# Kernel optimization log

Measured on AMD Instinct MI355X. Metric: run time of the kernel, lower is better.

## Reference

```python
import jax, jax.numpy as jnp
import numpy as np

S = 64.0
M = 0.5
COS_M = float(np.cos(M))
SIN_M = float(np.sin(M))
MM = float(np.sin(M) * M)
THRESHOLD = float(np.cos(np.pi - M))
B, D, V = 2048, 512, 100000


def setup_inputs() -> dict:
    key = jax.random.key(0)
    k1, k2, k3 = jax.random.split(key, 3)
    embeddings = jax.random.normal(k1, (B, D), dtype=jnp.float32)
    labels = jax.random.randint(k2, (B,), 0, V, dtype=jnp.int64)
    # xavier_uniform for [V, D]: limit = sqrt(6/(fan_in+fan_out))
    limit = float(np.sqrt(6.0 / (D + V)))
    weight = jax.random.uniform(k3, (V, D), minval=-limit, maxval=limit, dtype=jnp.float32)
    return {"embeddings": embeddings, "labels": labels, "weight": weight}


def _l2norm(x, axis):
    # matches F.normalize(p=2, eps=1e-12)
    n = jnp.linalg.norm(x, axis=axis, keepdims=True)
    return x / jnp.maximum(n, 1e-12)


def reference(embeddings, labels, weight):
    e = _l2norm(embeddings, axis=1)          # [B, D]
    w = _l2norm(weight, axis=1)              # [V, D]
    cos_theta = jnp.clip(e @ w.T, -1.0, 1.0)  # [B, V]
    sin_theta = jnp.sqrt(jnp.clip(1.0 - cos_theta * cos_theta, 0.0, 1.0))
    cos_theta_m = cos_theta * COS_M - sin_theta * SIN_M
    cos_theta_m = jnp.where(cos_theta > THRESHOLD, cos_theta_m, cos_theta - MM)
    logits = cos_theta_m * S
    logp = jax.nn.log_softmax(logits, axis=1)
    nll = -jnp.take_along_axis(logp, labels[:, None], axis=1)[:, 0]
    return jnp.mean(nll)
```

## Files before the change

kernel.cpp:

```cpp
#include <hip/hip_runtime.h>
#include <hip/hip_bf16.h>
#include <math.h>

#define B_ 2048
#define D_ 512
#define V_ 100000
#define BM 128
#define BN 128
#define NCT 782
#define NBLK (16 * NCT)
#define NBUF 3
#define RED_STRIDE 20

constexpr float S_SCALE = 64.0f;
constexpr float COS_M_ = 0.8775825618903728f;
constexpr float SIN_M_ = 0.479425538604203f;
constexpr float MM_    = 0.2397127693021015f;
constexpr float THRESH = -0.8775825618903728f;
constexpr float LOG2E  = 1.4426950408889634f;
constexpr float LN2    = 0.6931471805599453f;
constexpr float S2     = 64.0f * LOG2E;
constexpr float CMS2   = COS_M_ * S2;
constexpr float SINM_S2= SIN_M_ * S2;
constexpr float KS2    = SINM_S2 * SINM_S2;
constexpr float MMS2   = MM_ * S2;

constexpr float QS     = 508.0f;
constexpr float S8SQ   = QS * QS;
constexpr float S4_    = S8SQ * S8SQ;
constexpr float KS2C   = KS2 / S4_;
constexpr float CMS2C  = CMS2 / S8SQ;
constexpr float S2C    = S2 / S8SQ;
constexpr float THRESHI= THRESH * S8SQ;

constexpr float PA0  = -SINM_S2;
constexpr float PA1C = (SINM_S2 * 0.5f)    / S4_;
constexpr float PA2C = (SINM_S2 * 0.125f)  / (S4_ * S4_);
constexpr float PA3C = (SINM_S2 * 0.0625f) / (S4_ * S4_ * S4_);
constexpr float TH45I = 0.45f * S8SQ;

typedef __attribute__((ext_vector_type(8))) short short8;
typedef __attribute__((ext_vector_type(2))) float f32x2;
typedef __attribute__((ext_vector_type(4))) float f32x4;
typedef __attribute__((ext_vector_type(4))) int i32x4;

__device__ __forceinline__ unsigned short f2bf(float x) {
    __hip_bfloat16 h = __float2bfloat16(x);
    unsigned short u;
    __builtin_memcpy(&u, &h, 2);
    return u;
}

__device__ __forceinline__ void load_lds16(const void* g, void* l) {
    __builtin_amdgcn_global_load_lds(
        (const __attribute__((address_space(1))) unsigned int*)g,
        (__attribute__((address_space(3))) unsigned int*)l,
        16, 0, 0);
}

__device__ __forceinline__ int q8(float x) {
    float v = fminf(fmaxf(x * QS, -127.0f), 127.0f);
    return (int)rintf(v);
}
__device__ __forceinline__ unsigned int pk_i8x4(float x, float y, float z, float w) {
    return ((unsigned)q8(x) & 255u) | (((unsigned)q8(y) & 255u) << 8) |
           (((unsigned)q8(z) & 255u) << 16) | (((unsigned)q8(w) & 255u) << 24);
}

__global__ void k_norm_e(const float* __restrict__ e, unsigned short* __restrict__ ebf,
                         unsigned char* __restrict__ ebq, float* __restrict__ rne,
                         unsigned int* __restrict__ zbuf) {
    if (zbuf && blockIdx.x == 0) zbuf[threadIdx.x] = 0u;
    int row = blockIdx.x * 4 + (threadIdx.x >> 6);
    int lane = threadIdx.x & 63;
    const float4* src = (const float4*)(e + (size_t)row * D_);
    float4 a = src[lane];
    float4 b = src[lane + 64];
    float ss = a.x*a.x + a.y*a.y + a.z*a.z + a.w*a.w
             + b.x*b.x + b.y*b.y + b.z*b.z + b.w*b.w;
    #pragma unroll
    for (int d = 1; d < 64; d <<= 1) ss += __shfl_xor(ss, d, 64);
    float rn = 1.0f / fmaxf(sqrtf(ss), 1e-12f);
    ushort4* dst = (ushort4*)(ebf + (size_t)row * D_);
    dst[lane]      = make_ushort4(f2bf(a.x*rn), f2bf(a.y*rn), f2bf(a.z*rn), f2bf(a.w*rn));
    dst[lane + 64] = make_ushort4(f2bf(b.x*rn), f2bf(b.y*rn), f2bf(b.z*rn), f2bf(b.w*rn));
    if (ebq) {
        unsigned int* d8 = (unsigned int*)(ebq + (size_t)row * D_);
        d8[lane]      = pk_i8x4(a.x*rn, a.y*rn, a.z*rn, a.w*rn);
        d8[lane + 64] = pk_i8x4(b.x*rn, b.y*rn, b.z*rn, b.w*rn);
    }
    if (lane == 0) rne[row] = rn;
}

__global__ void k_norm_w(const float* __restrict__ w, float* __restrict__ rnw,
                         unsigned char* __restrict__ wbq) {
    int row = blockIdx.x * 4 + (threadIdx.x >> 6);
    int lane = threadIdx.x & 63;
    const float4* src = (const float4*)(w + (size_t)row * D_);
    float4 a = src[lane];
    float4 b = src[lane + 64];
    float ss = a.x*a.x + a.y*a.y + a.z*a.z + a.w*a.w
             + b.x*b.x + b.y*b.y + b.z*b.z + b.w*b.w;
    #pragma unroll
    for (int d = 1; d < 64; d <<= 1) ss += __shfl_xor(ss, d, 64);
    float rn = 1.0f / fmaxf(sqrtf(ss), 1e-12f);
    if (wbq) {
        unsigned int* d8 = (unsigned int*)(wbq + (size_t)row * D_);
        d8[lane]      = pk_i8x4(a.x*rn, a.y*rn, a.z*rn, a.w*rn);
        d8[lane + 64] = pk_i8x4(b.x*rn, b.y*rn, b.z*rn, b.w*rn);
    }
    if (lane == 0) rnw[row] = rn;
}

__global__ __launch_bounds__(256, 3) void k_gemm8(const unsigned char* __restrict__ ebq,
                                                  const unsigned char* __restrict__ wbq,
                                                  const unsigned char* __restrict__ zbuf,
                                                  float* __restrict__ partials) {
    const int id = blockIdx.x;
    const int wi = (id & 7) * (NBLK / 8) + (id >> 3);
    const int ct = wi >> 4, rt = wi & 15;
    const int row0 = rt * BM, n0 = ct * BN;
    const int tid = threadIdx.x, lane = tid & 63, wid = tid >> 6;
    const int wm = wid >> 1, wn = wid & 1;

    __shared__ __align__(16) unsigned char lds8[NBUF][16384];
    float* red = (float*)&lds8[0][0];

    i32x4 acc[4][4];
    #pragma unroll
    for (int i = 0; i < 4; ++i)
        #pragma unroll
        for (int j = 0; j < 4; ++j)
            acc[i][j] = (i32x4){0, 0, 0, 0};

    const int c_ = (lane & 3) ^ ((lane >> 3) & 3);
    const int r0s = wid * 16 + (lane >> 2);
    const unsigned char* gA0 = ebq + (size_t)(row0 + r0s) * D_ + c_ * 16;
    const unsigned char* gA1 = ebq + (size_t)(row0 + 64 + r0s) * D_ + c_ * 16;
    int gb0 = n0 + r0s, gb1 = n0 + 64 + r0s;
    const unsigned char* gB0 = (gb0 < V_) ? wbq + (size_t)gb0 * D_ + c_ * 16 : zbuf + c_ * 16;
    const unsigned char* gB1 = (gb1 < V_) ? wbq + (size_t)gb1 * D_ + c_ * 16 : zbuf + c_ * 16;
    const int lb = wid * 1024;

    auto STAGE = [&](int t) {
        unsigned char* Lb = &lds8[t % NBUF][0];
        const int off = t * 64;
        load_lds16(gA0 + off, Lb + lb);
        load_lds16(gA1 + off, Lb + 4096 + lb);
        load_lds16(gB0 + off, Lb + 8192 + lb);
        load_lds16(gB1 + off, Lb + 12288 + lb);
    };

    const int sA = ((lane >> 4) ^ ((lane >> 1) & 3)) & 3;
    int aoff[4], boff[4];
    #pragma unroll
    for (int mf = 0; mf < 4; ++mf)
        aoff[mf] = (wm * 64 + mf * 16 + (lane & 15)) * 64 + sA * 16;
    #pragma unroll
    for (int nf = 0; nf < 4; ++nf)
        boff[nf] = 8192 + (wn * 64 + nf * 16 + (lane & 15)) * 64 + sA * 16;

    STAGE(0);
    STAGE(1);
    for (int t = 0; t < 8; ++t) {
        if (t < 7) asm volatile("s_waitcnt vmcnt(4)\n\ts_barrier" ::: "memory");
        else       asm volatile("s_waitcnt vmcnt(0)\n\ts_barrier" ::: "memory");
        if (t + 2 < 8) STAGE(t + 2);

        const char* Lb = (const char*)&lds8[t % NBUF][0];
        i32x4 af[4], bq[4];
        #pragma unroll
        for (int mf = 0; mf < 4; ++mf) af[mf] = *(const i32x4*)(Lb + aoff[mf]);
        #pragma unroll
        for (int nf = 0; nf < 4; ++nf) bq[nf] = *(const i32x4*)(Lb + boff[nf]);
        #pragma unroll
        for (int mf = 0; mf < 4; ++mf)
            #pragma unroll
            for (int nf = 0; nf < 4; ++nf)
                acc[mf][nf] = __builtin_amdgcn_mfma_i32_16x16x64_i8(af[mf], bq[nf], acc[mf][nf], 0, 0, 0);
    }
    __syncthreads();

    const f32x2 k3 = {PA3C, PA3C}, k2 = {PA2C, PA2C}, k1 = {PA1C, PA1C},
                k0 = {PA0, PA0},   kc = {CMS2C, CMS2C};
    #pragma unroll
    for (int mf = 0; mf < 4; ++mf) {
        #pragma unroll
        for (int r = 0; r < 4; ++r) {
            float c0 = (float)acc[mf][0][r];
            float c1 = (float)acc[mf][1][r];
            float c2v = (float)acc[mf][2][r];
            float c3 = (float)acc[mf][3][r];
            float am = fmaxf(fmaxf(fabsf(c0), fabsf(c1)), fmaxf(fabsf(c2v), fabsf(c3)));
            float vsum;
            if (__builtin_expect(__any(am > TH45I), 0)) {
                float cs0 = c0, cs1 = c1, cs2 = c2v, cs3 = c3;
                vsum = 0.0f;
                float csa[4] = {cs0, cs1, cs2, cs3};
                #pragma unroll
                for (int nf = 0; nf < 4; ++nf) {
                    float ci = __builtin_amdgcn_fmed3f(csa[nf], -S8SQ, S8SQ);
                    float tt = fmaf(-ci, ci, S4_);
                    float sts = __builtin_amdgcn_sqrtf(tt * KS2C);
                    float lgm = fmaf(ci, CMS2C, -sts);
                    float lga = fmaf(ci, S2C, -MMS2);
                    float lg = (ci > THRESHI) ? lgm : lga;
                    vsum += __builtin_amdgcn_exp2f(lg);
                }
            } else {
                f32x2 ca = {c0, c1}, cb = {c2v, c3};
                f32x2 ua = ca * ca, ub = cb * cb;
                f32x2 pa = __builtin_elementwise_fma(ua, k3, k2);
                pa = __builtin_elementwise_fma(ua, pa, k1);
                pa = __builtin_elementwise_fma(ua, pa, k0);
                pa = __builtin_elementwise_fma(ca, kc, pa);
                f32x2 pb = __builtin_elementwise_fma(ub, k3, k2);
                pb = __builtin_elementwise_fma(ub, pb, k1);
                pb = __builtin_elementwise_fma(ub, pb, k0);
                pb = __builtin_elementwise_fma(cb, kc, pb);
                vsum = (__builtin_amdgcn_exp2f(pa.x) + __builtin_amdgcn_exp2f(pa.y))
                     + (__builtin_amdgcn_exp2f(pb.x) + __builtin_amdgcn_exp2f(pb.y));
            }
            int rowloc = wm * 64 + mf * 16 + (lane >> 4) * 4 + r;
            red[(wn * BM + rowloc) * RED_STRIDE + (lane & 15)] = vsum;
        }
    }
    __syncthreads();
    if (tid < BM) {
        const float4* p0 = (const float4*)(red + (size_t)tid * RED_STRIDE);
        const float4* p1 = (const float4*)(red + (size_t)(BM + tid) * RED_STRIDE);
        float s = 0.0f;
        #pragma unroll
        for (int q = 0; q < 4; ++q) {
            float4 u = p0[q], v = p1[q];
            s += (u.x + u.y) + (u.z + u.w) + (v.x + v.y) + (v.z + v.w);
        }
        partials[(size_t)ct * B_ + row0 + tid] = s;
    }
}

__device__ __forceinline__ int swz64(int row, int col) {
    return (row * 64 + col) ^ ((row & 7) << 3);
}
__global__ __launch_bounds__(256) void k_gemm_fb(const unsigned short* __restrict__ ebf,
                                                 const float* __restrict__ w,
                                                 const float* __restrict__ rnw,
                                                 float* __restrict__ partials) {
    const int rt = blockIdx.x, ct = blockIdx.y;
    const int row0 = rt * BM, n0 = ct * BN;
    const int tid = threadIdx.x, lane = tid & 63, wid = tid >> 6;
    const int wm = wid >> 1, wn = wid & 1;
    __shared__ __align__(16) unsigned short As[BM * 64];
    __shared__ __align__(16) unsigned short Bs[BN * 64];
    float* red = (float*)&As[0];
    f32x4 acc[4][4];
    #pragma unroll
    for (int i = 0; i < 4; ++i)
        #pragma unroll
        for (int j = 0; j < 4; ++j) acc[i][j] = (f32x4){0.f, 0.f, 0.f, 0.f};
    for (int ks = 0; ks < D_ / 64; ++ks) {
        const int kk = ks * 64;
        #pragma unroll
        for (int p = 0; p < 4; ++p) {
            int idx = p * 256 + tid;
            int r = idx >> 3, c = (idx & 7) * 8;
            *(uint4*)(As + swz64(r, c)) = *(const uint4*)(ebf + (size_t)(row0 + r) * D_ + kk + c);
        }
        #pragma unroll
        for (int p = 0; p < 4; ++p) {
            int idx = p * 256 + tid;
            int r = idx >> 3, c = (idx & 7) * 8;
            int gr = n0 + r;
            uint4 val = make_uint4(0, 0, 0, 0);
            if (gr < V_) {
                float rn = rnw[gr];
                const float4* src = (const float4*)(w + (size_t)gr * D_ + kk + c);
                float4 f0 = src[0], f1 = src[1];
                val.x = (unsigned)f2bf(f0.x*rn) | ((unsigned)f2bf(f0.y*rn) << 16);
                val.y = (unsigned)f2bf(f0.z*rn) | ((unsigned)f2bf(f0.w*rn) << 16);
                val.z = (unsigned)f2bf(f1.x*rn) | ((unsigned)f2bf(f1.y*rn) << 16);
                val.w = (unsigned)f2bf(f1.z*rn) | ((unsigned)f2bf(f1.w*rn) << 16);
            }
            *(uint4*)(Bs + swz64(r, c)) = val;
        }
        __syncthreads();
        #pragma unroll
        for (int kc = 0; kc < 2; ++kc) {
            const int kbase = kc * 32 + (lane >> 4) * 8;
            short8 af[4], bfr[4];
            #pragma unroll
            for (int mf = 0; mf < 4; ++mf) af[mf] = *(const short8*)(As + swz64(wm * 64 + mf * 16 + (lane & 15), kbase));
            #pragma unroll
            for (int nf = 0; nf < 4; ++nf) bfr[nf] = *(const short8*)(Bs + swz64(wn * 64 + nf * 16 + (lane & 15), kbase));
            #pragma unroll
            for (int mf = 0; mf < 4; ++mf)
                #pragma unroll
                for (int nf = 0; nf < 4; ++nf)
                    acc[mf][nf] = __builtin_amdgcn_mfma_f32_16x16x32_bf16(af[mf], bfr[nf], acc[mf][nf], 0, 0, 0);
        }
        __syncthreads();
    }
    const int vlim = V_ - n0;
    #pragma unroll
    for (int mf = 0; mf < 4; ++mf) {
        #pragma unroll
        for (int r = 0; r < 4; ++r) {
            float vsum = 0.0f;
            #pragma unroll
            for (int nf = 0; nf < 4; ++nf) {
                float c = acc[mf][nf][r];
                int coltile = wn * 64 + nf * 16 + (lane & 15);
                c = __builtin_amdgcn_fmed3f(c, -1.0f, 1.0f);
                float tt = fmaf(-c, c, 1.0f);
                float sts = __builtin_amdgcn_sqrtf(tt * KS2);
                float lgm = fmaf(c, CMS2, -sts);
                float lga = fmaf(c, S2, -MMS2);
                float lg = (c > THRESH) ? lgm : lga;
                lg = (coltile < vlim) ? lg : -INFINITY;
                vsum += __builtin_amdgcn_exp2f(lg);
            }
            int rowloc = wm * 64 + mf * 16 + (lane >> 4) * 4 + r;
            red[(wn * BM + rowloc) * RED_STRIDE + (lane & 15)] = vsum;
        }
    }
    __syncthreads();
    if (tid < BM) {
        const float4* p0 = (const float4*)(red + (size_t)tid * RED_STRIDE);
        const float4* p1 = (const float4*)(red + (size_t)(BM + tid) * RED_STRIDE);
        float s = 0.0f;
        #pragma unroll
        for (int q = 0; q < 4; ++q) {
            float4 u = p0[q], v = p1[q];
            s += (u.x + u.y) + (u.z + u.w) + (v.x + v.y) + (v.z + v.w);
        }
        partials[(size_t)ct * B_ + row0 + tid] = s;
    }
}

__device__ __forceinline__ int get_label(const int* lab32, int b) {
    bool is64 = true;
    #pragma unroll
    for (int i = 1; i < 16; i += 2) is64 = is64 && (lab32[i] == 0);
    return is64 ? (int)(((const long long*)lab32)[b]) : lab32[b];
}

__global__ void k_row(const float* __restrict__ e, const float* __restrict__ w,
                      const int* __restrict__ labels, const float* __restrict__ rne,
                      const float* __restrict__ rnw, const float* __restrict__ partials,
                      float* __restrict__ row_nll, float padcorr) {
    const int b = blockIdx.x;
    const int tid = threadIdx.x;

    float s = 0.0f;
    for (int ctn = tid; ctn < NCT; ctn += 256) s += partials[(size_t)ctn * B_ + b];
    #pragma unroll
    for (int d = 1; d < 64; d <<= 1) s += __shfl_xor(s, d, 64);
    __shared__ float ss_[4], sd_[4];
    if ((tid & 63) == 0) ss_[tid >> 6] = s;

    int lab = get_label(labels, b);
    const float* ep = e + (size_t)b * D_;
    const float* wp = w + (size_t)lab * D_;
    float dot = ep[tid] * wp[tid] + ep[tid + 256] * wp[tid + 256];
    #pragma unroll
    for (int d = 1; d < 64; d <<= 1) dot += __shfl_xor(dot, d, 64);
    if ((tid & 63) == 0) sd_[tid >> 6] = dot;
    __syncthreads();

    if (tid == 0) {
        float S = (ss_[0] + ss_[1]) + (ss_[2] + ss_[3]) - padcorr;
        float lse = __builtin_amdgcn_logf(S) * LN2;
        float c = (sd_[0] + sd_[1] + sd_[2] + sd_[3]) * rne[b] * rnw[lab];
        c = fminf(fmaxf(c, -1.0f), 1.0f);
        float st = sqrtf(fmaxf(1.0f - c * c, 0.0f));
        float cm = c * COS_M_ - st * SIN_M_;
        cm = (c > THRESH) ? cm : (c - MM_);
        row_nll[b] = lse - cm * S_SCALE;
    }
}

__global__ void k_mean(const float* __restrict__ row_nll, float* __restrict__ out) {
    int tid = threadIdx.x;
    float s = 0.0f;
    for (int i = tid; i < B_; i += 256) s += row_nll[i];
    #pragma unroll
    for (int d = 1; d < 64; d <<= 1) s += __shfl_xor(s, d, 64);
    __shared__ float sb[4];
    if ((tid & 63) == 0) sb[tid >> 6] = s;
    __syncthreads();
    if (tid == 0) out[0] = (sb[0] + sb[1] + sb[2] + sb[3]) / (float)B_;
}

extern "C" void kernel_launch(void* const* d_in, const int* in_sizes, int n_in,
                              void* d_out, int out_size, void* d_ws, size_t ws_size,
                              hipStream_t stream) {
    const float* e      = (const float*)d_in[0];
    const int*   labels = (const int*)d_in[1];
    const float* w      = (const float*)d_in[2];
    float* out = (float*)d_out;
    char* ws = (char*)d_ws;

    unsigned short* ebf = (unsigned short*)ws;
    float* rne          = (float*)(ws + 2097152);
    float* rnw          = (float*)(ws + 2105344);
    float* partials     = (float*)(ws + 2505344);
    float* row_nll      = (float*)(ws + 8911488);
    unsigned int* zbuf  = (unsigned int*)(ws + 8919680);
    unsigned char* ebq  = (unsigned char*)(ws + 8923776);
    unsigned char* wbq  = (unsigned char*)(ws + 9972352);
    const size_t NEED_PRE = 9972352 + (size_t)V_ * D_;

    const bool pre = ws_size >= NEED_PRE;
    const float padcorr = pre ? 96.0f * exp2f(-(float)SINM_S2) : 0.0f;

    k_norm_e<<<B_ / 4, 256, 0, stream>>>(e, ebf, pre ? ebq : nullptr, rne, pre ? zbuf : nullptr);
    k_norm_w<<<V_ / 4, 256, 0, stream>>>(w, rnw, pre ? wbq : nullptr);
    if (pre) {
        k_gemm8<<<NBLK, 256, 0, stream>>>(ebq, wbq, (const unsigned char*)zbuf, partials);
    } else {
        dim3 g3(B_ / BM, NCT);
        k_gemm_fb<<<g3, 256, 0, stream>>>(ebf, w, rnw, partials);
    }
    k_row<<<B_, 256, 0, stream>>>(e, w, labels, rne, rnw, partials, row_nll, padcorr);
    k_mean<<<1, 256, 0, stream>>>(row_nll, out);
}
```

Baseline: 194.1 us.

## Interleave split A/B prefetch with half-MFMA batches and raise wave priority

Splits the per-iteration global-to-LDS staging into separate A and B halves. Each half is issued between the LDS fragment reads and one half of the MFMA block, so memory traffic overlaps matrix work instead of all being issued at the top of the iteration. It also wraps each MFMA batch in s_setprio, adds sched_barrier fences, and adds a second workgroup barrier mid-iteration. The aim is better overlap of loads and MFMA issue across waves, at the cost of an extra barrier and explicit lgkmcnt waits per K step.

Result: no change. 194.4 us (+0.2%).

```diff
diff --git a/kernel.cpp b/kernel.cpp
--- a/kernel.cpp
+++ b/kernel.cpp
@@ -142,11 +142,15 @@
     const unsigned char* gB1 = (gb1 < V_) ? wbq + (size_t)gb1 * D_ + c_ * 16 : zbuf + c_ * 16;
     const int lb = wid * 1024;
 
-    auto STAGE = [&](int t) {
+    auto STAGE_A = [&](int t) {
         unsigned char* Lb = &lds8[t % NBUF][0];
         const int off = t * 64;
         load_lds16(gA0 + off, Lb + lb);
         load_lds16(gA1 + off, Lb + 4096 + lb);
+    };
+    auto STAGE_B = [&](int t) {
+        unsigned char* Lb = &lds8[t % NBUF][0];
+        const int off = t * 64;
         load_lds16(gB0 + off, Lb + 8192 + lb);
         load_lds16(gB1 + off, Lb + 12288 + lb);
     };
@@ -160,24 +164,44 @@
     for (int nf = 0; nf < 4; ++nf)
         boff[nf] = 8192 + (wn * 64 + nf * 16 + (lane & 15)) * 64 + sA * 16;
 
-    STAGE(0);
-    STAGE(1);
+    STAGE_A(0); STAGE_B(0);
+    STAGE_A(1); STAGE_B(1);
     for (int t = 0; t < 8; ++t) {
-        if (t < 7) asm volatile("s_waitcnt vmcnt(4)\n\ts_barrier" ::: "memory");
-        else       asm volatile("s_waitcnt vmcnt(0)\n\ts_barrier" ::: "memory");
-        if (t + 2 < 8) STAGE(t + 2);
+        if (t < 7) asm volatile("s_waitcnt vmcnt(4)" ::: "memory");
+        else       asm volatile("s_waitcnt vmcnt(0)" ::: "memory");
+        __builtin_amdgcn_s_barrier();
 
         const char* Lb = (const char*)&lds8[t % NBUF][0];
         i32x4 af[4], bq[4];
-        #pragma unroll
-        for (int mf = 0; mf < 4; ++mf) af[mf] = *(const i32x4*)(Lb + aoff[mf]);
+
         #pragma unroll
         for (int nf = 0; nf < 4; ++nf) bq[nf] = *(const i32x4*)(Lb + boff[nf]);
-        #pragma unroll
-        for (int mf = 0; mf < 4; ++mf)
+        af[0] = *(const i32x4*)(Lb + aoff[0]);
+        af[1] = *(const i32x4*)(Lb + aoff[1]);
+        if (t + 2 < 8) STAGE_A(t + 2);
+        asm volatile("s_waitcnt lgkmcnt(0)" ::: "memory");
+        __builtin_amdgcn_sched_barrier(0);
+        __builtin_amdgcn_s_setprio(1);
+        #pragma unroll
+        for (int mf = 0; mf < 2; ++mf)
             #pragma unroll
             for (int nf = 0; nf < 4; ++nf)
                 acc[mf][nf] = __builtin_amdgcn_mfma_i32_16x16x64_i8(af[mf], bq[nf], acc[mf][nf], 0, 0, 0);
+        __builtin_amdgcn_s_setprio(0);
+        __builtin_amdgcn_s_barrier();
+
+        af[2] = *(const i32x4*)(Lb + aoff[2]);
+        af[3] = *(const i32x4*)(Lb + aoff[3]);
+        if (t + 2 < 8) STAGE_B(t + 2);
+        asm volatile("s_waitcnt lgkmcnt(0)" ::: "memory");
+        __builtin_amdgcn_sched_barrier(0);
+        __builtin_amdgcn_s_setprio(1);
+        #pragma unroll
+        for (int mf = 2; mf < 4; ++mf)
+            #pragma unroll
+            for (int nf = 0; nf < 4; ++nf)
+                acc[mf][nf] = __builtin_amdgcn_mfma_i32_16x16x64_i8(af[mf], bq[nf], acc[mf][nf], 0, 0, 0);
+        __builtin_amdgcn_s_setprio(0);
     }
     __syncthreads();
 
@@ -194,9 +218,8 @@
             float am = fmaxf(fmaxf(fabsf(c0), fabsf(c1)), fmaxf(fabsf(c2v), fabsf(c3)));
             float vsum;
             if (__builtin_expect(__any(am > TH45I), 0)) {
-                float cs0 = c0, cs1 = c1, cs2 = c2v, cs3 = c3;
+                float csa[4] = {c0, c1, c2v, c3};
                 vsum = 0.0f;
-                float csa[4] = {cs0, cs1, cs2, cs3};
                 #pragma unroll
                 for (int nf = 0; nf < 4; ++nf) {
                     float ci = __builtin_amdgcn_fmed3f(csa[nf], -S8SQ, S8SQ);
```

## Enlarge int8 GEMM row tile to 256 and prioritize MFMA issue

Applied to the files above, without the earlier changes.

Doubles the M tile of the int8 GEMM from 128 to 256 rows, so each block loads one B (weight) tile and reuses it across twice as many embedding rows. This halves the block count and the repeated weight traffic, in exchange for doubled accumulator registers and a lower occupancy target (launch bounds 3 to 2). It also splits the wait and barrier, waits for all LDS reads before the MFMA loop, and raises wave priority during the MFMA block. The reduction LDS region grows to 256 rows, which fits inside the enlarged shared buffer.

New measurement: 193.8 us. No clear change (-0.1%).

```diff
diff --git a/kernel.cpp b/kernel.cpp
--- a/kernel.cpp
+++ b/kernel.cpp
@@ -7,8 +7,9 @@
 #define V_ 100000
 #define BM 128
 #define BN 128
+#define BMK 256
 #define NCT 782
-#define NBLK (16 * NCT)
+#define NBLK (8 * NCT)
 #define NBUF 3
 #define RED_STRIDE 20
 
@@ -112,31 +113,33 @@
     if (lane == 0) rnw[row] = rn;
 }
 
-__global__ __launch_bounds__(256, 3) void k_gemm8(const unsigned char* __restrict__ ebq,
+__global__ __launch_bounds__(256, 2) void k_gemm8(const unsigned char* __restrict__ ebq,
                                                   const unsigned char* __restrict__ wbq,
                                                   const unsigned char* __restrict__ zbuf,
                                                   float* __restrict__ partials) {
     const int id = blockIdx.x;
     const int wi = (id & 7) * (NBLK / 8) + (id >> 3);
-    const int ct = wi >> 4, rt = wi & 15;
-    const int row0 = rt * BM, n0 = ct * BN;
+    const int ct = wi >> 3, rt = wi & 7;
+    const int row0 = rt * BMK, n0 = ct * BN;
     const int tid = threadIdx.x, lane = tid & 63, wid = tid >> 6;
     const int wm = wid >> 1, wn = wid & 1;
 
-    __shared__ __align__(16) unsigned char lds8[NBUF][16384];
+    __shared__ __align__(16) unsigned char lds8[NBUF][24576];
     float* red = (float*)&lds8[0][0];
 
-    i32x4 acc[4][4];
-    #pragma unroll
-    for (int i = 0; i < 4; ++i)
+    i32x4 acc[8][4];
+    #pragma unroll
+    for (int i = 0; i < 8; ++i)
         #pragma unroll
         for (int j = 0; j < 4; ++j)
             acc[i][j] = (i32x4){0, 0, 0, 0};
 
     const int c_ = (lane & 3) ^ ((lane >> 3) & 3);
     const int r0s = wid * 16 + (lane >> 2);
-    const unsigned char* gA0 = ebq + (size_t)(row0 + r0s) * D_ + c_ * 16;
-    const unsigned char* gA1 = ebq + (size_t)(row0 + 64 + r0s) * D_ + c_ * 16;
+    const unsigned char* gA[4];
+    #pragma unroll
+    for (int i = 0; i < 4; ++i)
+        gA[i] = ebq + (size_t)(row0 + i * 64 + r0s) * D_ + c_ * 16;
     int gb0 = n0 + r0s, gb1 = n0 + 64 + r0s;
     const unsigned char* gB0 = (gb0 < V_) ? wbq + (size_t)gb0 * D_ + c_ * 16 : zbuf + c_ * 16;
     const unsigned char* gB1 = (gb1 < V_) ? wbq + (size_t)gb1 * D_ + c_ * 16 : zbuf + c_ * 16;
@@ -145,46 +148,53 @@
     auto STAGE = [&](int t) {
         unsigned char* Lb = &lds8[t % NBUF][0];
         const int off = t * 64;
-        load_lds16(gA0 + off, Lb + lb);
-        load_lds16(gA1 + off, Lb + 4096 + lb);
-        load_lds16(gB0 + off, Lb + 8192 + lb);
-        load_lds16(gB1 + off, Lb + 12288 + lb);
+        load_lds16(gA[0] + off, Lb + lb);
+        load_lds16(gA[1] + off, Lb + 4096 + lb);
+        load_lds16(gA[2] + off, Lb + 8192 + lb);
+        load_lds16(gA[3] + off, Lb + 12288 + lb);
+        load_lds16(gB0 + off, Lb + 16384 + lb);
+        load_lds16(gB1 + off, Lb + 20480 + lb);
     };
 
     const int sA = ((lane >> 4) ^ ((lane >> 1) & 3)) & 3;
-    int aoff[4], boff[4];
-    #pragma unroll
-    for (int mf = 0; mf < 4; ++mf)
-        aoff[mf] = (wm * 64 + mf * 16 + (lane & 15)) * 64 + sA * 16;
+    int aoff[8], boff[4];
+    #pragma unroll
+    for (int mf = 0; mf < 8; ++mf)
+        aoff[mf] = (wm * 128 + mf * 16 + (lane & 15)) * 64 + sA * 16;
     #pragma unroll
     for (int nf = 0; nf < 4; ++nf)
-        boff[nf] = 8192 + (wn * 64 + nf * 16 + (lane & 15)) * 64 + sA * 16;
+        boff[nf] = 16384 + (wn * 64 + nf * 16 + (lane & 15)) * 64 + sA * 16;
 
     STAGE(0);
     STAGE(1);
     for (int t = 0; t < 8; ++t) {
-        if (t < 7) asm volatile("s_waitcnt vmcnt(4)\n\ts_barrier" ::: "memory");
-        else       asm volatile("s_waitcnt vmcnt(0)\n\ts_barrier" ::: "memory");
+        if (t < 7) asm volatile("s_waitcnt vmcnt(6)" ::: "memory");
+        else       asm volatile("s_waitcnt vmcnt(0)" ::: "memory");
+        __builtin_amdgcn_s_barrier();
         if (t + 2 < 8) STAGE(t + 2);
 
         const char* Lb = (const char*)&lds8[t % NBUF][0];
-        i32x4 af[4], bq[4];
-        #pragma unroll
-        for (int mf = 0; mf < 4; ++mf) af[mf] = *(const i32x4*)(Lb + aoff[mf]);
+        i32x4 af[8], bq[4];
         #pragma unroll
         for (int nf = 0; nf < 4; ++nf) bq[nf] = *(const i32x4*)(Lb + boff[nf]);
         #pragma unroll
-        for (int mf = 0; mf < 4; ++mf)
+        for (int mf = 0; mf < 8; ++mf) af[mf] = *(const i32x4*)(Lb + aoff[mf]);
+        asm volatile("s_waitcnt lgkmcnt(0)" ::: "memory");
+        __builtin_amdgcn_sched_barrier(0);
+        __builtin_amdgcn_s_setprio(1);
+        #pragma unroll
+        for (int mf = 0; mf < 8; ++mf)
             #pragma unroll
             for (int nf = 0; nf < 4; ++nf)
                 acc[mf][nf] = __builtin_amdgcn_mfma_i32_16x16x64_i8(af[mf], bq[nf], acc[mf][nf], 0, 0, 0);
+        __builtin_amdgcn_s_setprio(0);
     }
     __syncthreads();
 
     const f32x2 k3 = {PA3C, PA3C}, k2 = {PA2C, PA2C}, k1 = {PA1C, PA1C},
                 k0 = {PA0, PA0},   kc = {CMS2C, CMS2C};
     #pragma unroll
-    for (int mf = 0; mf < 4; ++mf) {
+    for (int mf = 0; mf < 8; ++mf) {
         #pragma unroll
         for (int r = 0; r < 4; ++r) {
             float c0 = (float)acc[mf][0][r];
@@ -194,9 +204,8 @@
             float am = fmaxf(fmaxf(fabsf(c0), fabsf(c1)), fmaxf(fabsf(c2v), fabsf(c3)));
             float vsum;
             if (__builtin_expect(__any(am > TH45I), 0)) {
-                float cs0 = c0, cs1 = c1, cs2 = c2v, cs3 = c3;
+                float csa[4] = {c0, c1, c2v, c3};
                 vsum = 0.0f;
-                float csa[4] = {cs0, cs1, cs2, cs3};
                 #pragma unroll
                 for (int nf = 0; nf < 4; ++nf) {
                     float ci = __builtin_amdgcn_fmed3f(csa[nf], -S8SQ, S8SQ);
@@ -221,14 +230,14 @@
                 vsum = (__builtin_amdgcn_exp2f(pa.x) + __builtin_amdgcn_exp2f(pa.y))
                      + (__builtin_amdgcn_exp2f(pb.x) + __builtin_amdgcn_exp2f(pb.y));
             }
-            int rowloc = wm * 64 + mf * 16 + (lane >> 4) * 4 + r;
-            red[(wn * BM + rowloc) * RED_STRIDE + (lane & 15)] = vsum;
+            int rowloc = wm * 128 + mf * 16 + (lane >> 4) * 4 + r;
+            red[(wn * BMK + rowloc) * RED_STRIDE + (lane & 15)] = vsum;
         }
     }
     __syncthreads();
-    if (tid < BM) {
+    {
         const float4* p0 = (const float4*)(red + (size_t)tid * RED_STRIDE);
-        const float4* p1 = (const float4*)(red + (size_t)(BM + tid) * RED_STRIDE);
+        const float4* p1 = (const float4*)(red + (size_t)(BMK + tid) * RED_STRIDE);
         float s = 0.0f;
         #pragma unroll
         for (int q = 0; q < 4; ++q) {
```
